# Kernel optimization log

Measured on AMD Instinct MI355X. Metric: run time of the kernel, lower is better.

## Reference

```python
import jax, jax.numpy as jnp
import numpy as np

NHEADS = 16
SCALE_BASE = 512
GN_EPS = 1e-5


def rotate_every_two(x):
    x1 = x[..., ::2]
    x2 = x[..., 1::2]
    return jnp.stack((-x2, x1), axis=-1).reshape(x.shape)


def xpos_apply(x, downscale, offset=0):
    # x: [B, T, C]; XPOS over the FULL embedding dim (applied before head split)
    B, T, C = x.shape
    half = C // 2
    scale_vec = (jnp.arange(0, C, 2, dtype=jnp.float32) + 0.4 * C) / (1.4 * C)  # [half]
    min_pos = -(T + offset) // 2
    max_pos = T + offset + min_pos
    power = jnp.arange(min_pos, max_pos, dtype=jnp.float32) / SCALE_BASE  # [L]
    scale = scale_vec[None, :] ** power[:, None]  # [L, half]
    L = scale.shape[0]
    inv_freq = 1.0 / (10000.0 ** (jnp.arange(half, dtype=jnp.float32) / half))
    sinusoid = jnp.arange(L, dtype=jnp.float32)[:, None] * inv_freq[None, :]  # [L, half]
    sin, cos = jnp.sin(sinusoid), jnp.cos(sinusoid)
    if L > T:
        scale, sin, cos = scale[-T:], sin[-T:], cos[-T:]
    if downscale:
        scale = 1.0 / scale
    sin = jnp.repeat(sin * scale, 2, axis=-1)  # [T, C] (duplicate_interleave)
    cos = jnp.repeat(cos * scale, 2, axis=-1)
    return x * cos + rotate_every_two(x) * sin


def decay_mask(nheads, T):
    gamma = 1.0 - 2.0 ** (-5.0 - jnp.arange(nheads, dtype=jnp.float32))  # [H]
    idx = jnp.arange(T)
    diff = idx[:, None] - idx[None, :]  # [T, T]
    keep = diff >= 0
    m = gamma[:, None, None] ** jnp.where(keep, diff, 0).astype(jnp.float32)
    return jnp.where(keep[None, :, :], m, 0.0)  # [H, T, T]


def setup_inputs() -> dict:
    key = jax.random.key(0)
    ks = jax.random.split(key, 6)
    B, T, C = 2, 2048, 1024
    w_std = 0.02
    return {
        "x": jax.random.normal(ks[0], (B, T, C), jnp.float32),
        "w_qkvff": jax.random.normal(ks[1], (5 * C, C), jnp.float32) * w_std,
        "w_gated": jax.random.normal(ks[2], (C, C), jnp.float32) * w_std,
        "b_gated": jnp.zeros((C,), jnp.float32),
        "w_proj": jax.random.normal(ks[3], (C, C), jnp.float32) * w_std,
        "b_proj": jnp.zeros((C,), jnp.float32),
        "gn_w": jnp.ones((C,), jnp.float32),
        "gn_b": jnp.zeros((C,), jnp.float32),
        "w_ff": jax.random.normal(ks[4], (C, 2 * C), jnp.float32) * w_std,
        "rms_w": jnp.ones((C,), jnp.float32),
    }


def reference(x, w_qkvff, w_gated, b_gated, w_proj, b_proj, gn_w, gn_b, w_ff, rms_w):
    B, T, C = x.shape
    H = NHEADS
    hd = C // H
    # RMSNorm: x / clamp(||x|| * C^-0.5, 1e-8) * w
    nrm = jnp.sqrt(jnp.sum(x * x, axis=-1, keepdims=True)) * (C ** -0.5)
    x_ = x / jnp.maximum(nrm, 1e-8) * rms_w
    # fused qkvff projection (Linear, no bias): [B,T,5C]
    qkvff = jnp.einsum('btc,oc->bto', x_, w_qkvff)
    q, k, v, ff = jnp.split(qkvff, [C, 2 * C, 3 * C], axis=-1)
    q = xpos_apply(q, downscale=False)
    k = xpos_apply(k, downscale=True)
    # split heads -> [B,H,T,hd]
    q = q.reshape(B, T, H, hd).transpose(0, 2, 1, 3)
    k = k.reshape(B, T, H, hd).transpose(0, 2, 1, 3)
    v = v.reshape(B, T, H, hd).transpose(0, 2, 1, 3)
    # parallel retention: decay-masked QK^T @ V
    scores = jnp.einsum('bhtd,bhsd->bhts', q, k) * (hd ** -0.5)
    scores = scores * decay_mask(H, T)[None]
    y = jnp.einsum('bhts,bhsd->bhtd', scores, v)  # [B,H,T,hd]
    # GroupNorm(H groups) applied over flattened (B*T, C)
    yg = y.transpose(0, 2, 1, 3).reshape(B * T, H, hd)
    mu = jnp.mean(yg, axis=-1, keepdims=True)
    var = jnp.mean((yg - mu) ** 2, axis=-1, keepdims=True)
    yg = (yg - mu) / jnp.sqrt(var + GN_EPS)
    y = yg.reshape(B * T, C) * gn_w + gn_b
    y = y.reshape(B, T, C)
    # gated SiLU on raw x (pre-norm), then output proj
    y = jax.nn.silu(jnp.einsum('btc,oc->bto', x, w_gated) + b_gated) * y
    y = jnp.einsum('btc,oc->bto', y, w_proj) + b_proj
    # gated FFN branch: exact (erf) GELU then Linear(2C->C, no bias)
    ff_out = jnp.einsum('bte,ce->btc', jax.nn.gelu(ff, approximate=False), w_ff)
    return x + ff_out + y
```

## Files before the change

kernel.cpp:

```cpp
#include <hip/hip_runtime.h>
#include <math.h>

#define B_  2
#define T_  2048
#define C_  1024
#define H_  16
#define FC_ 5120

typedef __attribute__((ext_vector_type(8))) short  s16x8;
typedef __attribute__((ext_vector_type(4))) float  f32x4;
typedef __attribute__((ext_vector_type(2))) unsigned short u16x2;
typedef __attribute__((ext_vector_type(4))) unsigned short u16x4;
typedef __attribute__((ext_vector_type(8))) unsigned short u16x8;

__device__ __forceinline__ ushort f2bf(float f) {
    union { float f; unsigned u; } v; v.f = f;
    unsigned r = v.u + 0x7FFFu + ((v.u >> 16) & 1u);
    return (ushort)(r >> 16);
}

__global__ __launch_bounds__(256) void cvt_bf16_kernel(const float* __restrict__ src,
                                                       ushort* __restrict__ dst, int n8) {
    int i = blockIdx.x * 256 + threadIdx.x;
    if (i >= n8) return;
    float4 a = ((const float4*)src)[2*i];
    float4 b = ((const float4*)src)[2*i + 1];
    u16x8 o;
    o[0] = f2bf(a.x); o[1] = f2bf(a.y); o[2] = f2bf(a.z); o[3] = f2bf(a.w);
    o[4] = f2bf(b.x); o[5] = f2bf(b.y); o[6] = f2bf(b.z); o[7] = f2bf(b.w);
    *(u16x8*)(dst + 8*i) = o;
}

__global__ __launch_bounds__(256) void rmsnorm_kernel(const float* __restrict__ x,
                                                      const float* __restrict__ rms_w,
                                                      ushort* __restrict__ xn) {
    int row = blockIdx.x;
    int tid = threadIdx.x;
    float4 v = ((const float4*)(x + (size_t)row * C_))[tid];
    float ss = v.x*v.x + v.y*v.y + v.z*v.z + v.w*v.w;
    #pragma unroll
    for (int m = 32; m >= 1; m >>= 1) ss += __shfl_xor(ss, m);
    __shared__ float wsum[4];
    if ((tid & 63) == 0) wsum[tid >> 6] = ss;
    __syncthreads();
    float tot = wsum[0] + wsum[1] + wsum[2] + wsum[3];
    float nrm = sqrtf(tot) * 0.03125f;
    float inv = 1.0f / fmaxf(nrm, 1e-8f);
    float4 w = ((const float4*)rms_w)[tid];
    u16x4 o;
    o[0] = f2bf(v.x * inv * w.x);  o[1] = f2bf(v.y * inv * w.y);
    o[2] = f2bf(v.z * inv * w.z);  o[3] = f2bf(v.w * inv * w.w);
    *(u16x4*)(xn + (size_t)row * C_ + 4*tid) = o;
}

__global__ __launch_bounds__(256) void xpos_bf16_kernel(const float* __restrict__ qkvff,
                                                        ushort* __restrict__ qkv) {
    int bt = blockIdx.x;
    int t = bt & (T_ - 1);
    float tf = (float)t;
    const float* row = qkvff + (size_t)bt * FC_;
    ushort* orow = qkv + (size_t)bt * 3072;
    float power = (tf - 1024.0f) * (1.0f / 512.0f);
    for (int i = threadIdx.x; i < 512; i += 256) {
        float sv    = (2.0f * (float)i + 409.6f) * (1.0f / 1433.6f);
        float scale = exp2f(power * log2f(sv));
        float invf  = exp2f((float)i * (-13.287712379549449f / 512.0f));
        float ang   = tf * invf;
        float sn, cs;
        sincosf(ang, &sn, &cs);
        float rs = 1.0f / scale;
        int hh = i >> 5;
        float lg2g = log2f(1.0f - exp2f(-5.0f - (float)hh));
        float gq = exp2f(lg2g * tf) * 0.125f;
        float gk = exp2f(-lg2g * tf);
        float2 q = *(const float2*)(row + 2*i);
        float2 k = *(const float2*)(row + C_ + 2*i);
        float qox = (q.x*(cs*scale) - q.y*(sn*scale)) * gq;
        float qoy = (q.y*(cs*scale) + q.x*(sn*scale)) * gq;
        float kox = (k.x*(cs*rs) - k.y*(sn*rs)) * gk;
        float koy = (k.y*(cs*rs) + k.x*(sn*rs)) * gk;
        u16x2 qo; qo[0] = f2bf(qox); qo[1] = f2bf(qoy);
        u16x2 ko; ko[0] = f2bf(kox); ko[1] = f2bf(koy);
        *(u16x2*)(orow + 2*i) = qo;
        *(u16x2*)(orow + 1024 + 2*i) = ko;
    }
    {
        int c = threadIdx.x * 4;
        float4 v = *(const float4*)(row + 2*C_ + c);
        u16x4 o; o[0] = f2bf(v.x); o[1] = f2bf(v.y); o[2] = f2bf(v.z); o[3] = f2bf(v.w);
        *(u16x4*)(orow + 2048 + c) = o;
    }
}

__global__ __launch_bounds__(256) void gelu_bf16_kernel(const float* __restrict__ qkvff,
                                                        ushort* __restrict__ ffb) {
    const float* row = qkvff + (size_t)blockIdx.x * FC_ + 3*C_;
    ushort* orow = ffb + (size_t)blockIdx.x * 2048;
    for (int i = threadIdx.x; i < 512; i += 256) {
        float4 v = ((const float4*)row)[i];
        u16x4 o;
        o[0] = f2bf(0.5f * v.x * (1.0f + erff(v.x * 0.70710678118f)));
        o[1] = f2bf(0.5f * v.y * (1.0f + erff(v.y * 0.70710678118f)));
        o[2] = f2bf(0.5f * v.z * (1.0f + erff(v.z * 0.70710678118f)));
        o[3] = f2bf(0.5f * v.w * (1.0f + erff(v.w * 0.70710678118f)));
        *(u16x4*)(orow + 4*i) = o;
    }
}

template<int EPI>
__global__ __launch_bounds__(256) void gemm_bf16_kernel(
        const ushort* __restrict__ A, int lda,
        const ushort* __restrict__ W, int ldw,
        float* __restrict__ Cmat, int ldc, int K,
        const float* __restrict__ bias,
        const float* __restrict__ add1,
        const float* __restrict__ add2) {
    __shared__ __align__(16) ushort As[128*64];
    __shared__ __align__(16) ushort Bs[128*64];
    int tid = threadIdx.x;
    int m0 = blockIdx.y * 128, n0 = blockIdx.x * 128;
    int wave = tid >> 6, lane = tid & 63;
    int lo = lane & 15, hi = lane >> 4;
    int wm = (wave >> 1) * 64, wn = (wave & 1) * 64;
    int srow = tid >> 3;
    int su   = tid & 7;
    f32x4 acc[4][4] = {};

    u16x8 ra[4], rb[4];
    #pragma unroll
    for (int i = 0; i < 4; ++i) {
        int row = srow + 32*i;
        ra[i] = *(const u16x8*)(A + (size_t)(m0 + row) * lda + su*8);
        rb[i] = *(const u16x8*)(W + (size_t)(n0 + row) * ldw + su*8);
    }
    for (int k0 = 0;;) {
        __syncthreads();
        #pragma unroll
        for (int i = 0; i < 4; ++i) {
            int row = srow + 32*i;
            int off = row*128 + ((su*16) ^ ((row & 7) << 4));
            *(u16x8*)((char*)As + off) = ra[i];
            *(u16x8*)((char*)Bs + off) = rb[i];
        }
        __syncthreads();
        k0 += 64;
        if (k0 < K) {
            #pragma unroll
            for (int i = 0; i < 4; ++i) {
                int row = srow + 32*i;
                ra[i] = *(const u16x8*)(A + (size_t)(m0 + row) * lda + k0 + su*8);
                rb[i] = *(const u16x8*)(W + (size_t)(n0 + row) * ldw + k0 + su*8);
            }
        }
        #pragma unroll
        for (int kc = 0; kc < 2; ++kc) {
            s16x8 af[4], bf[4];
            #pragma unroll
            for (int g = 0; g < 4; ++g) {
                int arow = wm + g*16 + lo;
                af[g] = *(const s16x8*)((const char*)As +
                         arow*128 + ((kc*64 + hi*16) ^ ((arow & 7) << 4)));
                int brow = wn + g*16 + lo;
                bf[g] = *(const s16x8*)((const char*)Bs +
                         brow*128 + ((kc*64 + hi*16) ^ ((brow & 7) << 4)));
            }
            #pragma unroll
            for (int mg = 0; mg < 4; ++mg)
                #pragma unroll
                for (int ng = 0; ng < 4; ++ng)
                    acc[mg][ng] = __builtin_amdgcn_mfma_f32_16x16x32_bf16(
                        af[mg], bf[ng], acc[mg][ng], 0, 0, 0);
        }
        if (k0 >= K) break;
    }
    #pragma unroll
    for (int mg = 0; mg < 4; ++mg) {
        #pragma unroll
        for (int r = 0; r < 4; ++r) {
            size_t m = (size_t)(m0 + wm + mg*16 + hi*4 + r);
            #pragma unroll
            for (int ng = 0; ng < 4; ++ng) {
                int n = n0 + wn + ng*16 + lo;
                float v = acc[mg][ng][r];
                if (EPI == 1) {
                    float s = v + bias[n];
                    v = s / (1.0f + expf(-s));
                } else if (EPI == 2) {
                    v += bias[n] + add1[m*ldc + n] + add2[m*ldc + n];
                }
                Cmat[m*ldc + n] = v;
            }
        }
    }
}

__global__ __launch_bounds__(256) void attn_mfma_kernel(const ushort* __restrict__ qkv,
                                                        float* __restrict__ y) {
    __shared__ ushort Ks[64*64];
    __shared__ ushort Vt[64*64];
    __shared__ ushort Ss[4][16*64];
    int tt = 31 - (int)blockIdx.x;
    int h = blockIdx.y, b = blockIdx.z;
    int t0 = tt * 64;
    int tid = threadIdx.x;
    int wave = tid >> 6, lane = tid & 63;
    int lo = lane & 15, hi = lane >> 4;
    const size_t bT = (size_t)b * T_;

    s16x8 qf0, qf1;
    {
        const ushort* qrow = qkv + (bT + t0 + wave*16 + lo) * 3072 + h*64;
        qf0 = *(const s16x8*)(qrow + hi*8);
        qf1 = *(const s16x8*)(qrow + 32 + hi*8);
    }
    f32x4 accy[4] = {};

    int kr = tid >> 2, kc = tid & 3;
    int vd0 = (tid & 15) * 4, vs0 = (tid >> 4) * 4;

    for (int st = 0; st <= tt; ++st) {
        int s0 = st * 64;
        __syncthreads();
        {
            const ushort* src = qkv + (bT + s0 + kr) * 3072 + 1024 + h*64;
            u16x8 a = *(const u16x8*)(src + kc*8);
            u16x8 c2 = *(const u16x8*)(src + (kc+4)*8);
            int base = kr * 128, sw = (kr & 7) << 4;
            *(u16x8*)((char*)Ks + ((base + kc*16) ^ sw))     = a;
            *(u16x8*)((char*)Ks + ((base + (kc+4)*16) ^ sw)) = c2;
        }
        {
            const ushort* src = qkv + (bT + s0 + vs0) * 3072 + 2048 + h*64 + vd0;
            u16x4 l0 = *(const u16x4*)(src);
            u16x4 l1 = *(const u16x4*)(src + 3072);
            u16x4 l2 = *(const u16x4*)(src + 2*3072);
            u16x4 l3 = *(const u16x4*)(src + 3*3072);
            #pragma unroll
            for (int i = 0; i < 4; ++i) {
                u16x4 o; o[0] = l0[i]; o[1] = l1[i]; o[2] = l2[i]; o[3] = l3[i];
                int d = vd0 + i;
                *(u16x4*)((char*)Vt + ((d*128 + vs0*2) ^ ((d & 7) << 4))) = o;
            }
        }
        __syncthreads();
        f32x4 sacc[4] = {};
        #pragma unroll
        for (int sn = 0; sn < 4; ++sn) {
            int srow = sn*16 + lo;
            int rb = srow * 128, sw = (srow & 7) << 4;
            s16x8 kf0 = *(const s16x8*)((const char*)Ks + ((rb + hi*16) ^ sw));
            s16x8 kf1 = *(const s16x8*)((const char*)Ks + ((rb + 64 + hi*16) ^ sw));
            sacc[sn] = __builtin_amdgcn_mfma_f32_16x16x32_bf16(qf0, kf0, sacc[sn], 0, 0, 0);
            sacc[sn] = __builtin_amdgcn_mfma_f32_16x16x32_bf16(qf1, kf1, sacc[sn], 0, 0, 0);
        }
        #pragma unroll
        for (int sn = 0; sn < 4; ++sn) {
            int sl = sn*16 + lo;
            #pragma unroll
            for (int r = 0; r < 4; ++r) {
                float v = sacc[sn][r];
                if (st == tt && sl > wave*16 + hi*4 + r) v = 0.0f;
                int tq = hi*4 + r;
                *(ushort*)((char*)Ss[wave] + ((tq*128 + sl*2) ^ ((tq & 7) << 4))) = f2bf(v);
            }
        }
        s16x8 sa0 = *(const s16x8*)((const char*)Ss[wave] + ((lo*128 + hi*16) ^ ((lo & 7) << 4)));
        s16x8 sa1 = *(const s16x8*)((const char*)Ss[wave] + ((lo*128 + 64 + hi*16) ^ ((lo & 7) << 4)));
        #pragma unroll
        for (int dn = 0; dn < 4; ++dn) {
            int d = dn*16 + lo;
            int rb = d * 128, sw = (d & 7) << 4;
            s16x8 vf0 = *(const s16x8*)((const char*)Vt + ((rb + hi*16) ^ sw));
            s16x8 vf1 = *(const s16x8*)((const char*)Vt + ((rb + 64 + hi*16) ^ sw));
            accy[dn] = __builtin_amdgcn_mfma_f32_16x16x32_bf16(sa0, vf0, accy[dn], 0, 0, 0);
            accy[dn] = __builtin_amdgcn_mfma_f32_16x16x32_bf16(sa1, vf1, accy[dn], 0, 0, 0);
        }
    }
    #pragma unroll
    for (int dn = 0; dn < 4; ++dn) {
        #pragma unroll
        for (int r = 0; r < 4; ++r) {
            int t = t0 + wave*16 + hi*4 + r;
            y[(bT + t) * C_ + h*64 + dn*16 + lo] = accy[dn][r];
        }
    }
}

__global__ __launch_bounds__(256) void gn_gate_kernel(const float* __restrict__ y,
                                                      const float* __restrict__ gate,
                                                      const float* __restrict__ gn_w,
                                                      const float* __restrict__ gn_b,
                                                      ushort* __restrict__ ygb) {
    int bt = blockIdx.x;
    int tid = threadIdx.x;
    float4 v = ((const float4*)(y + (size_t)bt * C_))[tid];
    float s1 = v.x + v.y + v.z + v.w;
    float s2 = v.x*v.x + v.y*v.y + v.z*v.z + v.w*v.w;
    #pragma unroll
    for (int m = 1; m < 16; m <<= 1) { s1 += __shfl_xor(s1, m); s2 += __shfl_xor(s2, m); }
    float mu   = s1 * (1.0f/64.0f);
    float var  = s2 * (1.0f/64.0f) - mu*mu;
    float rstd = rsqrtf(var + 1e-5f);
    float4 w  = ((const float4*)gn_w)[tid];
    float4 bb = ((const float4*)gn_b)[tid];
    float4 g  = ((const float4*)(gate + (size_t)bt * C_))[tid];
    u16x4 o;
    o[0] = f2bf(((v.x - mu)*rstd*w.x + bb.x) * g.x);
    o[1] = f2bf(((v.y - mu)*rstd*w.y + bb.y) * g.y);
    o[2] = f2bf(((v.z - mu)*rstd*w.z + bb.z) * g.z);
    o[3] = f2bf(((v.w - mu)*rstd*w.w + bb.w) * g.w);
    *(u16x4*)(ygb + (size_t)bt * C_ + 4*tid) = o;
}

extern "C" void kernel_launch(void* const* d_in, const int* in_sizes, int n_in,
                              void* d_out, int out_size, void* d_ws, size_t ws_size,
                              hipStream_t stream) {
    (void)in_sizes; (void)n_in; (void)out_size; (void)ws_size;
    const float* x       = (const float*)d_in[0];
    const float* w_qkvff = (const float*)d_in[1];
    const float* w_gated = (const float*)d_in[2];
    const float* b_gated = (const float*)d_in[3];
    const float* w_proj  = (const float*)d_in[4];
    const float* b_proj  = (const float*)d_in[5];
    const float* gn_w    = (const float*)d_in[6];
    const float* gn_b    = (const float*)d_in[7];
    const float* w_ff    = (const float*)d_in[8];
    const float* rms_w   = (const float*)d_in[9];
    float* out = (float*)d_out;

    const size_t NTOK = (size_t)B_ * T_;
    float* buf0  = (float*)d_ws;
    float* buf1  = buf0 + NTOK * C_;
    float* buf2  = buf1 + NTOK * C_;
    float* qkvff = buf2 + NTOK * C_;
    ushort* qkvb = (ushort*)(qkvff + NTOK * FC_);
    ushort* xb   = qkvb + NTOK * 3072;
    ushort* xnb  = xb + NTOK * C_;
    ushort* ffb  = xnb + NTOK * C_;
    ushort* ygb  = ffb + NTOK * 2048;
    ushort* wqb  = ygb + NTOK * C_;
    ushort* wgb  = wqb + (size_t)FC_ * C_;
    ushort* wpb  = wgb + (size_t)C_ * C_;
    ushort* wfb  = wpb + (size_t)C_ * C_;

    cvt_bf16_kernel<<<2048, 256, 0, stream>>>(x, xb, 524288);
    cvt_bf16_kernel<<<2560, 256, 0, stream>>>(w_qkvff, wqb, 655360);
    cvt_bf16_kernel<<<512,  256, 0, stream>>>(w_gated, wgb, 131072);
    cvt_bf16_kernel<<<512,  256, 0, stream>>>(w_proj,  wpb, 131072);
    cvt_bf16_kernel<<<1024, 256, 0, stream>>>(w_ff,    wfb, 262144);
    rmsnorm_kernel<<<4096, 256, 0, stream>>>(x, rms_w, xnb);
    gemm_bf16_kernel<0><<<dim3(40, 32), 256, 0, stream>>>(xnb, C_, wqb, C_, qkvff, FC_, C_,
                                                          nullptr, nullptr, nullptr);
    xpos_bf16_kernel<<<4096, 256, 0, stream>>>(qkvff, qkvb);
    gelu_bf16_kernel<<<4096, 256, 0, stream>>>(qkvff, ffb);
    attn_mfma_kernel<<<dim3(32, 16, 2), 256, 0, stream>>>(qkvb, buf1);
    gemm_bf16_kernel<1><<<dim3(8, 32), 256, 0, stream>>>(xb, C_, wgb, C_, buf2, C_, C_,
                                                         b_gated, nullptr, nullptr);
    gn_gate_kernel<<<4096, 256, 0, stream>>>(buf1, buf2, gn_w, gn_b, ygb);
    gemm_bf16_kernel<0><<<dim3(8, 32), 256, 0, stream>>>(ffb, 2*C_, wfb, 2*C_, buf0, C_, 2*C_,
                                                         nullptr, nullptr, nullptr);
    gemm_bf16_kernel<2><<<dim3(8, 32), 256, 0, stream>>>(ygb, C_, wpb, C_, out, C_, C_,
                                                         b_proj, x, buf0);
}
```

Before: 349.2 us.

## Fuse QKV GEMM epilogue to bf16 with GELU, pair attention tiles, narrow GEMM tiles

The QKV/FF GEMM now writes bf16 outputs directly: q/k go to a temporary, v goes straight into the packed qkv buffer, and the FF part gets exact GELU applied in the epilogue. This removes the fp32 qkvff round trip and the separate GELU kernel. The attention kernel pairs a short and a long causal row tile per block to balance work across blocks, and double-buffers K/V tiles in shared memory so the next tile's loads overlap compute. The 1024-wide GEMMs switch to 64-column tiles, doubling the block count on the small problems at the cost of less reuse per block.

```diff
diff --git a/kernel.cpp b/kernel.cpp
--- a/kernel.cpp
+++ b/kernel.cpp
@@ -17,6 +17,9 @@
     union { float f; unsigned u; } v; v.f = f;
     unsigned r = v.u + 0x7FFFu + ((v.u >> 16) & 1u);
     return (ushort)(r >> 16);
+}
+__device__ __forceinline__ float bf2f(ushort u) {
+    union { unsigned u; float f; } v; v.u = (unsigned)u << 16; return v.f;
 }
 
 __global__ __launch_bounds__(256) void cvt_bf16_kernel(const float* __restrict__ src,
@@ -53,12 +56,12 @@
     *(u16x4*)(xn + (size_t)row * C_ + 4*tid) = o;
 }
 
-__global__ __launch_bounds__(256) void xpos_bf16_kernel(const float* __restrict__ qkvff,
+__global__ __launch_bounds__(256) void xpos_bf16_kernel(const ushort* __restrict__ qktmp,
                                                         ushort* __restrict__ qkv) {
     int bt = blockIdx.x;
     int t = bt & (T_ - 1);
     float tf = (float)t;
-    const float* row = qkvff + (size_t)bt * FC_;
+    const ushort* row = qktmp + (size_t)bt * 2048;
     ushort* orow = qkv + (size_t)bt * 3072;
     float power = (tf - 1024.0f) * (1.0f / 512.0f);
     for (int i = threadIdx.x; i < 512; i += 256) {
@@ -73,93 +76,93 @@
         float lg2g = log2f(1.0f - exp2f(-5.0f - (float)hh));
         float gq = exp2f(lg2g * tf) * 0.125f;
         float gk = exp2f(-lg2g * tf);
-        float2 q = *(const float2*)(row + 2*i);
-        float2 k = *(const float2*)(row + C_ + 2*i);
-        float qox = (q.x*(cs*scale) - q.y*(sn*scale)) * gq;
-        float qoy = (q.y*(cs*scale) + q.x*(sn*scale)) * gq;
-        float kox = (k.x*(cs*rs) - k.y*(sn*rs)) * gk;
-        float koy = (k.y*(cs*rs) + k.x*(sn*rs)) * gk;
+        u16x2 qi = *(const u16x2*)(row + 2*i);
+        u16x2 ki = *(const u16x2*)(row + 1024 + 2*i);
+        float qx = bf2f(qi[0]), qy = bf2f(qi[1]);
+        float kx = bf2f(ki[0]), ky = bf2f(ki[1]);
+        float qox = (qx*(cs*scale) - qy*(sn*scale)) * gq;
+        float qoy = (qy*(cs*scale) + qx*(sn*scale)) * gq;
+        float kox = (kx*(cs*rs) - ky*(sn*rs)) * gk;
+        float koy = (ky*(cs*rs) + kx*(sn*rs)) * gk;
         u16x2 qo; qo[0] = f2bf(qox); qo[1] = f2bf(qoy);
         u16x2 ko; ko[0] = f2bf(kox); ko[1] = f2bf(koy);
         *(u16x2*)(orow + 2*i) = qo;
         *(u16x2*)(orow + 1024 + 2*i) = ko;
     }
-    {
-        int c = threadIdx.x * 4;
-        float4 v = *(const float4*)(row + 2*C_ + c);
-        u16x4 o; o[0] = f2bf(v.x); o[1] = f2bf(v.y); o[2] = f2bf(v.z); o[3] = f2bf(v.w);
-        *(u16x4*)(orow + 2048 + c) = o;
-    }
-}
-
-__global__ __launch_bounds__(256) void gelu_bf16_kernel(const float* __restrict__ qkvff,
-                                                        ushort* __restrict__ ffb) {
-    const float* row = qkvff + (size_t)blockIdx.x * FC_ + 3*C_;
-    ushort* orow = ffb + (size_t)blockIdx.x * 2048;
-    for (int i = threadIdx.x; i < 512; i += 256) {
-        float4 v = ((const float4*)row)[i];
-        u16x4 o;
-        o[0] = f2bf(0.5f * v.x * (1.0f + erff(v.x * 0.70710678118f)));
-        o[1] = f2bf(0.5f * v.y * (1.0f + erff(v.y * 0.70710678118f)));
-        o[2] = f2bf(0.5f * v.z * (1.0f + erff(v.z * 0.70710678118f)));
-        o[3] = f2bf(0.5f * v.w * (1.0f + erff(v.w * 0.70710678118f)));
-        *(u16x4*)(orow + 4*i) = o;
-    }
-}
-
-template<int EPI>
+}
+
+template<int EPI, int BN>
 __global__ __launch_bounds__(256) void gemm_bf16_kernel(
         const ushort* __restrict__ A, int lda,
         const ushort* __restrict__ W, int ldw,
         float* __restrict__ Cmat, int ldc, int K,
         const float* __restrict__ bias,
         const float* __restrict__ add1,
-        const float* __restrict__ add2) {
+        const float* __restrict__ add2,
+        ushort* __restrict__ oqk,
+        ushort* __restrict__ ov,
+        ushort* __restrict__ offb) {
+    constexpr int NG = BN / 32;
     __shared__ __align__(16) ushort As[128*64];
-    __shared__ __align__(16) ushort Bs[128*64];
+    __shared__ __align__(16) ushort Bs[BN*64];
     int tid = threadIdx.x;
-    int m0 = blockIdx.y * 128, n0 = blockIdx.x * 128;
+    int m0 = blockIdx.y * 128, n0 = blockIdx.x * BN;
     int wave = tid >> 6, lane = tid & 63;
     int lo = lane & 15, hi = lane >> 4;
-    int wm = (wave >> 1) * 64, wn = (wave & 1) * 64;
-    int srow = tid >> 3;
-    int su   = tid & 7;
-    f32x4 acc[4][4] = {};
+    int wm = (wave >> 1) * 64, wn = (wave & 1) * (BN/2);
+    int sra = tid >> 3, sua = tid & 7;
+    f32x4 acc[4][NG] = {};
 
     u16x8 ra[4], rb[4];
-    #pragma unroll
-    for (int i = 0; i < 4; ++i) {
-        int row = srow + 32*i;
-        ra[i] = *(const u16x8*)(A + (size_t)(m0 + row) * lda + su*8);
-        rb[i] = *(const u16x8*)(W + (size_t)(n0 + row) * ldw + su*8);
-    }
+    auto loadA = [&](int k0) {
+        #pragma unroll
+        for (int i = 0; i < 4; ++i)
+            ra[i] = *(const u16x8*)(A + (size_t)(m0 + sra + 32*i) * lda + k0 + sua*8);
+    };
+    auto loadB = [&](int k0) {
+        if constexpr (BN == 128) {
+            #pragma unroll
+            for (int i = 0; i < 4; ++i)
+                rb[i] = *(const u16x8*)(W + (size_t)(n0 + sra + 32*i) * ldw + k0 + sua*8);
+        } else {
+            int r = tid >> 2, c = tid & 3;
+            rb[0] = *(const u16x8*)(W + (size_t)(n0 + r) * ldw + k0 + c*8);
+            rb[1] = *(const u16x8*)(W + (size_t)(n0 + r) * ldw + k0 + (c+4)*8);
+        }
+    };
+    loadA(0); loadB(0);
     for (int k0 = 0;;) {
         __syncthreads();
         #pragma unroll
         for (int i = 0; i < 4; ++i) {
-            int row = srow + 32*i;
-            int off = row*128 + ((su*16) ^ ((row & 7) << 4));
-            *(u16x8*)((char*)As + off) = ra[i];
-            *(u16x8*)((char*)Bs + off) = rb[i];
+            int row = sra + 32*i;
+            *(u16x8*)((char*)As + (row*128 + ((sua*16) ^ ((row & 7) << 4)))) = ra[i];
+        }
+        if constexpr (BN == 128) {
+            #pragma unroll
+            for (int i = 0; i < 4; ++i) {
+                int row = sra + 32*i;
+                *(u16x8*)((char*)Bs + (row*128 + ((sua*16) ^ ((row & 7) << 4)))) = rb[i];
+            }
+        } else {
+            int r = tid >> 2, c = tid & 3, sw = (r & 7) << 4;
+            *(u16x8*)((char*)Bs + (r*128 + ((c*16) ^ sw)))     = rb[0];
+            *(u16x8*)((char*)Bs + (r*128 + (((c+4)*16) ^ sw))) = rb[1];
         }
         __syncthreads();
         k0 += 64;
-        if (k0 < K) {
-            #pragma unroll
-            for (int i = 0; i < 4; ++i) {
-                int row = srow + 32*i;
-                ra[i] = *(const u16x8*)(A + (size_t)(m0 + row) * lda + k0 + su*8);
-                rb[i] = *(const u16x8*)(W + (size_t)(n0 + row) * ldw + k0 + su*8);
-            }
-        }
+        if (k0 < K) { loadA(k0); loadB(k0); }
         #pragma unroll
         for (int kc = 0; kc < 2; ++kc) {
-            s16x8 af[4], bf[4];
+            s16x8 af[4], bf[NG];
             #pragma unroll
             for (int g = 0; g < 4; ++g) {
                 int arow = wm + g*16 + lo;
                 af[g] = *(const s16x8*)((const char*)As +
                          arow*128 + ((kc*64 + hi*16) ^ ((arow & 7) << 4)));
+            }
+            #pragma unroll
+            for (int g = 0; g < NG; ++g) {
                 int brow = wn + g*16 + lo;
                 bf[g] = *(const s16x8*)((const char*)Bs +
                          brow*128 + ((kc*64 + hi*16) ^ ((brow & 7) << 4)));
@@ -167,7 +170,7 @@
             #pragma unroll
             for (int mg = 0; mg < 4; ++mg)
                 #pragma unroll
-                for (int ng = 0; ng < 4; ++ng)
+                for (int ng = 0; ng < NG; ++ng)
                     acc[mg][ng] = __builtin_amdgcn_mfma_f32_16x16x32_bf16(
                         af[mg], bf[ng], acc[mg][ng], 0, 0, 0);
         }
@@ -179,109 +182,130 @@
         for (int r = 0; r < 4; ++r) {
             size_t m = (size_t)(m0 + wm + mg*16 + hi*4 + r);
             #pragma unroll
-            for (int ng = 0; ng < 4; ++ng) {
+            for (int ng = 0; ng < NG; ++ng) {
                 int n = n0 + wn + ng*16 + lo;
                 float v = acc[mg][ng][r];
-                if (EPI == 1) {
-                    float s = v + bias[n];
-                    v = s / (1.0f + expf(-s));
-                } else if (EPI == 2) {
-                    v += bias[n] + add1[m*ldc + n] + add2[m*ldc + n];
+                if constexpr (EPI == 3) {
+                    if (n0 < 2048)      oqk[m*2048 + n] = f2bf(v);
+                    else if (n0 < 3072) ov[m*3072 + n] = f2bf(v);
+                    else offb[m*2048 + (n - 3072)] =
+                             f2bf(0.5f * v * (1.0f + erff(v * 0.70710678118f)));
+                } else {
+                    if (EPI == 1) {
+                        float s = v + bias[n];
+                        v = s / (1.0f + expf(-s));
+                    } else if (EPI == 2) {
+                        v += bias[n] + add1[m*ldc + n] + add2[m*ldc + n];
+                    }
+                    Cmat[m*ldc + n] = v;
                 }
-                Cmat[m*ldc + n] = v;
-            }
-        }
-    }
-}
-
-__global__ __launch_bounds__(256) void attn_mfma_kernel(const ushort* __restrict__ qkv,
-                                                        float* __restrict__ y) {
-    __shared__ ushort Ks[64*64];
-    __shared__ ushort Vt[64*64];
+            }
+        }
+    }
+}
+
+__global__ __launch_bounds__(256) void attn_mfma2_kernel(const ushort* __restrict__ qkv,
+                                                         float* __restrict__ y) {
+    __shared__ ushort Ks[2][64*64];
+    __shared__ ushort Vt[2][64*64];
     __shared__ ushort Ss[4][16*64];
-    int tt = 31 - (int)blockIdx.x;
-    int h = blockIdx.y, b = blockIdx.z;
-    int t0 = tt * 64;
+    int F = blockIdx.x;
+    int o = (F & 7) * 64 + (F >> 3);
+    int tta = o & 15;
+    int h   = (o >> 4) & 15;
+    int b   = o >> 8;
+    int ttb = 31 - tta;
+    int t0a = tta * 64, t0b = ttb * 64;
     int tid = threadIdx.x;
     int wave = tid >> 6, lane = tid & 63;
     int lo = lane & 15, hi = lane >> 4;
     const size_t bT = (size_t)b * T_;
 
-    s16x8 qf0, qf1;
-    {
-        const ushort* qrow = qkv + (bT + t0 + wave*16 + lo) * 3072 + h*64;
-        qf0 = *(const s16x8*)(qrow + hi*8);
-        qf1 = *(const s16x8*)(qrow + 32 + hi*8);
-    }
-    f32x4 accy[4] = {};
+    const ushort* qra = qkv + (bT + t0a + wave*16 + lo) * 3072 + h*64;
+    const ushort* qrb = qkv + (bT + t0b + wave*16 + lo) * 3072 + h*64;
+    s16x8 qa0 = *(const s16x8*)(qra + hi*8);
+    s16x8 qa1 = *(const s16x8*)(qra + 32 + hi*8);
+    s16x8 qb0 = *(const s16x8*)(qrb + hi*8);
+    s16x8 qb1 = *(const s16x8*)(qrb + 32 + hi*8);
+    f32x4 acca[4] = {}, accb[4] = {};
 
     int kr = tid >> 2, kc = tid & 3;
     int vd0 = (tid & 15) * 4, vs0 = (tid >> 4) * 4;
-
-    for (int st = 0; st <= tt; ++st) {
-        int s0 = st * 64;
+    u16x8 rka, rkb;
+    u16x4 rv0, rv1, rv2, rv3;
+    auto loadt = [&](int s0) {
+        const ushort* src = qkv + (bT + s0 + kr) * 3072 + 1024 + h*64;
+        rka = *(const u16x8*)(src + kc*8);
+        rkb = *(const u16x8*)(src + (kc+4)*8);
+        const ushort* vsrc = qkv + (bT + s0 + vs0) * 3072 + 2048 + h*64 + vd0;
+        rv0 = *(const u16x4*)(vsrc);
+        rv1 = *(const u16x4*)(vsrc + 3072);
+        rv2 = *(const u16x4*)(vsrc + 2*3072);
+        rv3 = *(const u16x4*)(vsrc + 3*3072);
+    };
+    int cur = 0;
+    loadt(0);
+    for (int st = 0; st <= ttb; ++st) {
+        {
+            int base = kr * 128, sw = (kr & 7) << 4;
+            *(u16x8*)((char*)Ks[cur] + ((base + kc*16) ^ sw))     = rka;
+            *(u16x8*)((char*)Ks[cur] + ((base + (kc+4)*16) ^ sw)) = rkb;
+            #pragma unroll
+            for (int i = 0; i < 4; ++i) {
+                u16x4 o4; o4[0] = rv0[i]; o4[1] = rv1[i]; o4[2] = rv2[i]; o4[3] = rv3[i];
+                int d = vd0 + i;
+                *(u16x4*)((char*)Vt[cur] + ((d*128 + vs0*2) ^ ((d & 7) << 4))) = o4;
+            }
+        }
         __syncthreads();
-        {
-            const ushort* src = qkv + (bT + s0 + kr) * 3072 + 1024 + h*64;
-            u16x8 a = *(const u16x8*)(src + kc*8);
-            u16x8 c2 = *(const u16x8*)(src + (kc+4)*8);
-            int base = kr * 128, sw = (kr & 7) << 4;
-            *(u16x8*)((char*)Ks + ((base + kc*16) ^ sw))     = a;
-            *(u16x8*)((char*)Ks + ((base + (kc+4)*16) ^ sw)) = c2;
-        }
-        {
-            const ushort* src = qkv + (bT + s0 + vs0) * 3072 + 2048 + h*64 + vd0;
-            u16x4 l0 = *(const u16x4*)(src);
-            u16x4 l1 = *(const u16x4*)(src + 3072);
-            u16x4 l2 = *(const u16x4*)(src + 2*3072);
-            u16x4 l3 = *(const u16x4*)(src + 3*3072);
-            #pragma unroll
-            for (int i = 0; i < 4; ++i) {
-                u16x4 o; o[0] = l0[i]; o[1] = l1[i]; o[2] = l2[i]; o[3] = l3[i];
-                int d = vd0 + i;
-                *(u16x4*)((char*)Vt + ((d*128 + vs0*2) ^ ((d & 7) << 4))) = o;
-            }
-        }
-        __syncthreads();
-        f32x4 sacc[4] = {};
-        #pragma unroll
-        for (int sn = 0; sn < 4; ++sn) {
-            int srow = sn*16 + lo;
-            int rb = srow * 128, sw = (srow & 7) << 4;
-            s16x8 kf0 = *(const s16x8*)((const char*)Ks + ((rb + hi*16) ^ sw));
-            s16x8 kf1 = *(const s16x8*)((const char*)Ks + ((rb + 64 + hi*16) ^ sw));
-            sacc[sn] = __builtin_amdgcn_mfma_f32_16x16x32_bf16(qf0, kf0, sacc[sn], 0, 0, 0);
-            sacc[sn] = __builtin_amdgcn_mfma_f32_16x16x32_bf16(qf1, kf1, sacc[sn], 0, 0, 0);
-        }
-        #pragma unroll
-        for (int sn = 0; sn < 4; ++sn) {
-            int sl = sn*16 + lo;
-            #pragma unroll
-            for (int r = 0; r < 4; ++r) {
-                float v = sacc[sn][r];
-                if (st == tt && sl > wave*16 + hi*4 + r) v = 0.0f;
-                int tq = hi*4 + r;
-                *(ushort*)((char*)Ss[wave] + ((tq*128 + sl*2) ^ ((tq & 7) << 4))) = f2bf(v);
-            }
-        }
-        s16x8 sa0 = *(const s16x8*)((const char*)Ss[wave] + ((lo*128 + hi*16) ^ ((lo & 7) << 4)));
-        s16x8 sa1 = *(const s16x8*)((const char*)Ss[wave] + ((lo*128 + 64 + hi*16) ^ ((lo & 7) << 4)));
-        #pragma unroll
-        for (int dn = 0; dn < 4; ++dn) {
-            int d = dn*16 + lo;
-            int rb = d * 128, sw = (d & 7) << 4;
-            s16x8 vf0 = *(const s16x8*)((const char*)Vt + ((rb + hi*16) ^ sw));
-            s16x8 vf1 = *(const s16x8*)((const char*)Vt + ((rb + 64 + hi*16) ^ sw));
-            accy[dn] = __builtin_amdgcn_mfma_f32_16x16x32_bf16(sa0, vf0, accy[dn], 0, 0, 0);
-            accy[dn] = __builtin_amdgcn_mfma_f32_16x16x32_bf16(sa1, vf1, accy[dn], 0, 0, 0);
-        }
+        if (st < ttb) loadt((st + 1) * 64);
+
+        auto compute = [&](s16x8 q0, s16x8 q1, f32x4* accy, bool diag) {
+            f32x4 sacc[4] = {};
+            #pragma unroll
+            for (int sn = 0; sn < 4; ++sn) {
+                int srow = sn*16 + lo;
+                int rb2 = srow * 128, sw = (srow & 7) << 4;
+                s16x8 kf0 = *(const s16x8*)((const char*)Ks[cur] + ((rb2 + hi*16) ^ sw));
+                s16x8 kf1 = *(const s16x8*)((const char*)Ks[cur] + ((rb2 + 64 + hi*16) ^ sw));
+                sacc[sn] = __builtin_amdgcn_mfma_f32_16x16x32_bf16(q0, kf0, sacc[sn], 0, 0, 0);
+                sacc[sn] = __builtin_amdgcn_mfma_f32_16x16x32_bf16(q1, kf1, sacc[sn], 0, 0, 0);
+            }
+            #pragma unroll
+            for (int sn = 0; sn < 4; ++sn) {
+                int sl = sn*16 + lo;
+                #pragma unroll
+                for (int r = 0; r < 4; ++r) {
+                    float v = sacc[sn][r];
+                    if (diag && sl > wave*16 + hi*4 + r) v = 0.0f;
+                    int tq = hi*4 + r;
+                    *(ushort*)((char*)Ss[wave] + ((tq*128 + sl*2) ^ ((tq & 7) << 4))) = f2bf(v);
+                }
+            }
+            s16x8 sa0 = *(const s16x8*)((const char*)Ss[wave] + ((lo*128 + hi*16) ^ ((lo & 7) << 4)));
+            s16x8 sa1 = *(const s16x8*)((const char*)Ss[wave] + ((lo*128 + 64 + hi*16) ^ ((lo & 7) << 4)));
+            #pragma unroll
+            for (int dn = 0; dn < 4; ++dn) {
+                int d = dn*16 + lo;
+                int rb2 = d * 128, sw = (d & 7) << 4;
+                s16x8 vf0 = *(const s16x8*)((const char*)Vt[cur] + ((rb2 + hi*16) ^ sw));
+                s16x8 vf1 = *(const s16x8*)((const char*)Vt[cur] + ((rb2 + 64 + hi*16) ^ sw));
+                accy[dn] = __builtin_amdgcn_mfma_f32_16x16x32_bf16(sa0, vf0, accy[dn], 0, 0, 0);
+                accy[dn] = __builtin_amdgcn_mfma_f32_16x16x32_bf16(sa1, vf1, accy[dn], 0, 0, 0);
+            }
+        };
+        compute(qb0, qb1, accb, st == ttb);
+        if (st <= tta) compute(qa0, qa1, acca, st == tta);
+        cur ^= 1;
     }
     #pragma unroll
     for (int dn = 0; dn < 4; ++dn) {
         #pragma unroll
         for (int r = 0; r < 4; ++r) {
-            int t = t0 + wave*16 + hi*4 + r;
-            y[(bT + t) * C_ + h*64 + dn*16 + lo] = accy[dn][r];
+            int ta = t0a + wave*16 + hi*4 + r;
+            int tb = t0b + wave*16 + hi*4 + r;
+            y[(bT + ta) * C_ + h*64 + dn*16 + lo] = acca[dn][r];
+            y[(bT + tb) * C_ + h*64 + dn*16 + lo] = accb[dn][r];
         }
     }
 }
@@ -329,19 +353,19 @@
     float* out = (float*)d_out;
 
     const size_t NTOK = (size_t)B_ * T_;
-    float* buf0  = (float*)d_ws;
-    float* buf1  = buf0 + NTOK * C_;
-    float* buf2  = buf1 + NTOK * C_;
-    float* qkvff = buf2 + NTOK * C_;
-    ushort* qkvb = (ushort*)(qkvff + NTOK * FC_);
-    ushort* xb   = qkvb + NTOK * 3072;
-    ushort* xnb  = xb + NTOK * C_;
-    ushort* ffb  = xnb + NTOK * C_;
-    ushort* ygb  = ffb + NTOK * 2048;
-    ushort* wqb  = ygb + NTOK * C_;
-    ushort* wgb  = wqb + (size_t)FC_ * C_;
-    ushort* wpb  = wgb + (size_t)C_ * C_;
-    ushort* wfb  = wpb + (size_t)C_ * C_;
+    float* buf0   = (float*)d_ws;
+    float* buf1   = buf0 + NTOK * C_;
+    float* buf2   = buf1 + NTOK * C_;
+    ushort* qkvb  = (ushort*)(buf2 + NTOK * C_);
+    ushort* qktmp = qkvb + NTOK * 3072;
+    ushort* xb    = qktmp + NTOK * 2048;
+    ushort* xnb   = xb + NTOK * C_;
+    ushort* ffb   = xnb + NTOK * C_;
+    ushort* ygb   = ffb + NTOK * 2048;
+    ushort* wqb   = ygb + NTOK * C_;
+    ushort* wgb   = wqb + (size_t)FC_ * C_;
+    ushort* wpb   = wgb + (size_t)C_ * C_;
+    ushort* wfb   = wpb + (size_t)C_ * C_;
 
     cvt_bf16_kernel<<<2048, 256, 0, stream>>>(x, xb, 524288);
     cvt_bf16_kernel<<<2560, 256, 0, stream>>>(w_qkvff, wqb, 655360);
@@ -349,16 +373,15 @@
     cvt_bf16_kernel<<<512,  256, 0, stream>>>(w_proj,  wpb, 131072);
     cvt_bf16_kernel<<<1024, 256, 0, stream>>>(w_ff,    wfb, 262144);
     rmsnorm_kernel<<<4096, 256, 0, stream>>>(x, rms_w, xnb);
-    gemm_bf16_kernel<0><<<dim3(40, 32), 256, 0, stream>>>(xnb, C_, wqb, C_, qkvff, FC_, C_,
-                                                          nullptr, nullptr, nullptr);
-    xpos_bf16_kernel<<<4096, 256, 0, stream>>>(qkvff, qkvb);
-    gelu_bf16_kernel<<<4096, 256, 0, stream>>>(qkvff, ffb);
-    attn_mfma_kernel<<<dim3(32, 16, 2), 256, 0, stream>>>(qkvb, buf1);
-    gemm_bf16_kernel<1><<<dim3(8, 32), 256, 0, stream>>>(xb, C_, wgb, C_, buf2, C_, C_,
-                                                         b_gated, nullptr, nullptr);
+    gemm_bf16_kernel<3,128><<<dim3(40, 32), 256, 0, stream>>>(
+        xnb, C_, wqb, C_, nullptr, 0, C_, nullptr, nullptr, nullptr, qktmp, qkvb, ffb);
+    xpos_bf16_kernel<<<4096, 256, 0, stream>>>(qktmp, qkvb);
+    attn_mfma2_kernel<<<512, 256, 0, stream>>>(qkvb, buf1);
+    gemm_bf16_kernel<1,64><<<dim3(16, 32), 256, 0, stream>>>(
+        xb, C_, wgb, C_, buf2, C_, C_, b_gated, nullptr, nullptr, nullptr, nullptr, nullptr);
     gn_gate_kernel<<<4096, 256, 0, stream>>>(buf1, buf2, gn_w, gn_b, ygb);
-    gemm_bf16_kernel<0><<<dim3(8, 32), 256, 0, stream>>>(ffb, 2*C_, wfb, 2*C_, buf0, C_, 2*C_,
-                                                         nullptr, nullptr, nullptr);
-    gemm_bf16_kernel<2><<<dim3(8, 32), 256, 0, stream>>>(ygb, C_, wpb, C_, out, C_, C_,
-                                                         b_proj, x, buf0);
-}
+    gemm_bf16_kernel<0,64><<<dim3(16, 32), 256, 0, stream>>>(
+        ffb, 2*C_, wfb, 2*C_, buf0, C_, 2*C_, nullptr, nullptr, nullptr, nullptr, nullptr, nullptr);
+    gemm_bf16_kernel<2,64><<<dim3(16, 32), 256, 0, stream>>>(
+        ygb, C_, wpb, C_, out, C_, C_, b_proj, x, buf0, nullptr, nullptr, nullptr);
+}
```

New measurement: 324.4 us. 7.1% less time.
